# Optimization experiments

Measured on AMD Instinct MI355X. Metric: run time of the kernel, lower is better.

The kernel has to match this reference:

```python
import jax, jax.numpy as jnp
import numpy as np


def setup_inputs() -> dict:
    key = jax.random.key(0)
    k1, k2, k3 = jax.random.split(key, 3)
    B, C_IN, C_OUT, R, K = 4, 64, 64, 64, 3
    x = jax.random.normal(k1, (B, C_IN, R, R, R), dtype=jnp.float32)
    # per-voxel nonzero test |x|.sum(channel) != 0 used by the module)
    keep = jax.random.uniform(k2, (B, 1, R, R, R)) < 0.3
    x = x * keep.astype(jnp.float32)
    weight = jax.random.normal(k3, (C_OUT, C_IN, K, K, K), dtype=jnp.float32)
    return {"x": x, "weight": weight}


def reference(x, weight):
    # The torch module gathers a k^3 neighborhood at every nonzero input voxel,
    # contracts with the (unflipped) weight, and scatters to the same voxel.
    # This is exactly cross-correlation (torch conv semantics) with SAME padding,
    # masked to voxels where the input is nonzero across channels.
    K = weight.shape[-1]
    pad_l = K // 2
    pad_r = K - 1 - pad_l
    out = jax.lax.conv_general_dilated(
        x, weight,
        window_strides=(1, 1, 1),
        padding=[(pad_l, pad_r)] * 3,
        dimension_numbers=("NCDHW", "OIDHW", "NCDHW"),
    )  # [B, C_out, D, H, W]
    mask = (jnp.abs(x).sum(axis=1, keepdims=True) != 0)  # [B,1,D,H,W]
    return out * mask.astype(out.dtype)
```

## Files before the change

### kernel.cpp

```cpp
#include <hip/hip_runtime.h>
#include <stdint.h>


#define R3 262144
#define NVOX (4 * R3)
#define WSW_ELEMS (27 * 2 * 4 * 64 * 8)

typedef __attribute__((ext_vector_type(4))) float f32x4;
typedef __attribute__((ext_vector_type(8))) short short8;

static __device__ inline unsigned short f2bf(float f) {
    union { float f; unsigned u; } v; v.f = f;
    unsigned u = v.u;
    return (unsigned short)((u + 0x7fffu + ((u >> 16) & 1u)) >> 16);
}

__global__ void wprep(const float* __restrict__ w, unsigned short* __restrict__ wsw) {
    int e = blockIdx.x * 256 + threadIdx.x;
    if (e >= WSW_ELEMS) return;
    int j    = e & 7;
    int lane = (e >> 3) & 63;
    int nt   = (e >> 9) & 3;
    int kc   = (e >> 11) & 1;
    int tap  = e >> 12;
    int co = nt * 16 + (lane & 15);
    int ci = kc * 32 + ((lane >> 4) * 8) + j;
    wsw[e] = f2bf(w[(co * 64 + ci) * 27 + tap]);
}

__global__ void __launch_bounds__(256) xprep(const float* __restrict__ x,
                                             unsigned int* __restrict__ xt_u32,
                                             int* __restrict__ list,
                                             int* __restrict__ count) {
    __shared__ unsigned int lds[256 * 33];
    __shared__ unsigned int wcnt[4], wbase[4], bbase;
    int t = threadIdx.x;
    int v = blockIdx.x * 256 + t;
    int b = v >> 18;
    int s = v & (R3 - 1);
    const float* xb = x + (size_t)b * (64 * R3) + s;
    bool active = false;
#pragma unroll
    for (int c2 = 0; c2 < 32; ++c2) {
        float f0 = xb[(size_t)(2 * c2) * R3];
        float f1 = xb[(size_t)(2 * c2 + 1) * R3];
        active |= (f0 != 0.f) | (f1 != 0.f);
        lds[t * 33 + c2] = (unsigned)f2bf(f0) | ((unsigned)f2bf(f1) << 16);
    }
    __syncthreads();
    unsigned int* dst = xt_u32 + (size_t)blockIdx.x * 8192;
#pragma unroll
    for (int i = 0; i < 32; ++i) {
        int g = i * 256 + t;
        dst[g] = lds[(g >> 5) * 33 + (g & 31)];
    }
    int lane = t & 63, w = t >> 6;
    unsigned long long bal = __ballot(active);
    if (lane == 0) wcnt[w] = (unsigned)__popcll(bal);
    __syncthreads();
    if (t == 0) {
        unsigned tot = 0;
        for (int i = 0; i < 4; ++i) { wbase[i] = tot; tot += wcnt[i]; }
        bbase = (unsigned)atomicAdd(count, (int)tot);
    }
    __syncthreads();
    if (active) {
        unsigned pos = bbase + wbase[w] + (unsigned)__popcll(bal & ((1ULL << lane) - 1ULL));
        list[pos] = v;
    }
}

__global__ void __launch_bounds__(256) sconv_gemm(const unsigned short* __restrict__ xt,
                                                  const unsigned short* __restrict__ wsw,
                                                  const int* __restrict__ list,
                                                  const int* __restrict__ count_p,
                                                  float* __restrict__ out) {
    __shared__ __align__(16) unsigned short Alds[64 * 72];
    __shared__ int vids[64];
    int count = *count_p;
    int base = blockIdx.x * 64;
    if (base >= count) return;
    int t = threadIdx.x;
    if (t < 64) {
        int idx = base + t;
        vids[t] = (idx < count) ? list[idx] : -1;
    }
    __syncthreads();

    int lane = t & 63, w = t >> 6;
    int mt0 = (w & 1) * 2, nt0 = (w >> 1) * 2;
    f32x4 acc[2][2] = {};

    int srow = t >> 2;
    int scol = t & 3;
    int vid = vids[srow];
    bool vvalid = vid >= 0;
    int vx = vid & 63, vy = (vid >> 6) & 63, vz = (vid >> 12) & 63;
    int vbase = vid & ~(R3 - 1);

    for (int tap = 0; tap < 27; ++tap) {
        int dz = tap / 9 - 1, dy = (tap / 3) % 3 - 1, dx = tap % 3 - 1;
        uint4 val0 = {0, 0, 0, 0}, val1 = {0, 0, 0, 0};
        if (vvalid) {
            int nz = vz + dz, ny = vy + dy, nx = vx + dx;
            if ((unsigned)nz < 64u && (unsigned)ny < 64u && (unsigned)nx < 64u) {
                long long ns = (long long)vbase + nz * 4096 + ny * 64 + nx;
                const uint4* src = (const uint4*)(xt + (size_t)ns * 64) + scol * 2;
                val0 = src[0];
                val1 = src[1];
            }
        }
        *(uint4*)&Alds[srow * 72 + scol * 16] = val0;
        *(uint4*)&Alds[srow * 72 + scol * 16 + 8] = val1;
        __syncthreads();

#pragma unroll
        for (int kc = 0; kc < 2; ++kc) {
            short8 bfr[2], afr[2];
#pragma unroll
            for (int n = 0; n < 2; ++n) {
                int nt = nt0 + n;
                bfr[n] = *(const short8*)(wsw +
                          (((size_t)(tap * 8 + kc * 4 + nt)) * 64 + lane) * 8);
            }
#pragma unroll
            for (int m = 0; m < 2; ++m) {
                int row = (mt0 + m) * 16 + (lane & 15);
                afr[m] = *(const short8*)&Alds[row * 72 + kc * 32 + (lane >> 4) * 8];
            }
#pragma unroll
            for (int m = 0; m < 2; ++m)
#pragma unroll
                for (int n = 0; n < 2; ++n)
                    acc[m][n] = __builtin_amdgcn_mfma_f32_16x16x32_bf16(
                        afr[m], bfr[n], acc[m][n], 0, 0, 0);
        }
        __syncthreads();
    }

    int q = lane >> 4;
#pragma unroll
    for (int m = 0; m < 2; ++m) {
#pragma unroll
        for (int rg = 0; rg < 4; ++rg) {
            int row = (mt0 + m) * 16 + q * 4 + rg;
            if (base + row < count) {
                int vv = vids[row];
                int bb = vv >> 18;
                int sp = vv & (R3 - 1);
#pragma unroll
                for (int n = 0; n < 2; ++n) {
                    int co = (nt0 + n) * 16 + (lane & 15);
                    out[((size_t)(bb * 64 + co)) * R3 + sp] = acc[m][n][rg];
                }
            }
        }
    }
}

__global__ void __launch_bounds__(64) fallback_conv(const float* __restrict__ x,
                                                    const float* __restrict__ wt,
                                                    float* __restrict__ out) {
    __shared__ float rowb[66];
    int bid = blockIdx.x;
    int y = bid & 63, z = (bid >> 6) & 63, co = (bid >> 12) & 63, b = bid >> 18;
    int t = threadIdx.x;
    float acc = 0.f;
    bool active = false;
    for (int ci = 0; ci < 64; ++ci) {
        const float* xp = x + ((size_t)(b * 64 + ci)) * R3;
        const float* wp = wt + ((size_t)(co * 64 + ci)) * 27;
        for (int dz = -1; dz <= 1; ++dz) {
            int nz = z + dz;
            bool okz = (unsigned)nz < 64u;
            for (int dy = -1; dy <= 1; ++dy) {
                int ny = y + dy;
                bool ok = okz && ((unsigned)ny < 64u);
                float v = ok ? xp[nz * 4096 + ny * 64 + t] : 0.f;
                rowb[t + 1] = v;
                if (t == 0) { rowb[0] = 0.f; rowb[65] = 0.f; }
                __syncthreads();
                if (dz == 0 && dy == 0) active |= (rowb[t + 1] != 0.f);
                const float* wq = wp + (dz + 1) * 9 + (dy + 1) * 3;
                acc += rowb[t] * wq[0] + rowb[t + 1] * wq[1] + rowb[t + 2] * wq[2];
                __syncthreads();
            }
        }
    }
    out[((size_t)(b * 64 + co)) * R3 + z * 4096 + y * 64 + t] = active ? acc : 0.f;
}

extern "C" void kernel_launch(void* const* d_in, const int* in_sizes, int n_in,
                              void* d_out, int out_size, void* d_ws, size_t ws_size,
                              hipStream_t stream) {
    const float* x = (const float*)d_in[0];
    const float* w = (const float*)d_in[1];
    float* out = (float*)d_out;

    const size_t XT_BYTES  = (size_t)NVOX * 64 * 2;
    const size_t LIST_OFF  = XT_BYTES;
    const size_t WSW_OFF   = LIST_OFF + (size_t)NVOX * 4;
    const size_t CNT_OFF   = WSW_OFF + (size_t)WSW_ELEMS * 2;
    const size_t NEED      = CNT_OFF + 256;

    if (ws_size < NEED) {
        fallback_conv<<<NVOX, 64, 0, stream>>>(x, w, out);
        return;
    }

    unsigned int*   xt   = (unsigned int*)d_ws;
    int*            list = (int*)((char*)d_ws + LIST_OFF);
    unsigned short* wsw  = (unsigned short*)((char*)d_ws + WSW_OFF);
    int*            cnt  = (int*)((char*)d_ws + CNT_OFF);

    hipMemsetAsync(cnt, 0, sizeof(int), stream);
    hipMemsetAsync(d_out, 0, (size_t)out_size * sizeof(float), stream);
    wprep<<<WSW_ELEMS / 256, 256, 0, stream>>>(w, wsw);
    xprep<<<NVOX / 256, 256, 0, stream>>>(x, xt, list, cnt);
    sconv_gemm<<<NVOX / 64, 256, 0, stream>>>((const unsigned short*)xt, wsw, list, cnt, out);
}
```

Before: 710.8 us.

## Pad voxel grid with zero halo and double-buffer async LDS loads in sparse conv GEMM

Stores the bf16 channel-last input in a 66^3 zero-padded grid, adding a halo_zero kernel, so the gather needs no bounds checks. The GEMM kernel grows to 128 voxels per block with each warp covering all 64 output channels. It double-buffers the A and B tiles in LDS using global_load_lds with an XOR swizzle, so the next tap's loads overlap the current tap's MFMAs. This costs a larger workspace, an extra halo-zeroing pass, and more LDS per block.

```diff
diff --git a/kernel.cpp b/kernel.cpp
--- a/kernel.cpp
+++ b/kernel.cpp
@@ -4,6 +4,9 @@
 
 #define R3 262144
 #define NVOX (4 * R3)
+#define P  66
+#define PS (66 * 66)
+#define PB (66 * 66 * 66)
 #define WSW_ELEMS (27 * 2 * 4 * 64 * 8)
 
 typedef __attribute__((ext_vector_type(4))) float f32x4;
@@ -13,6 +16,12 @@
     union { float f; unsigned u; } v; v.f = f;
     unsigned u = v.u;
     return (unsigned short)((u + 0x7fffu + ((u >> 16) & 1u)) >> 16);
+}
+
+static __device__ __forceinline__ void gload16(const void* g, void* l) {
+    __builtin_amdgcn_global_load_lds(
+        (const __attribute__((address_space(1))) unsigned int*)g,
+        (__attribute__((address_space(3))) unsigned int*)l, 16, 0, 0);
 }
 
 __global__ void wprep(const float* __restrict__ w, unsigned short* __restrict__ wsw) {
@@ -28,11 +37,26 @@
     wsw[e] = f2bf(w[(co * 64 + ci) * 27 + tap]);
 }
 
+__global__ void __launch_bounds__(256) halo_zero(uint4* __restrict__ xt4) {
+    int p = blockIdx.x * 256 + threadIdx.x;
+    if (p >= 4 * PB) return;
+    int b = p / PB;
+    int rp = p - b * PB;
+    int z = rp / PS; rp -= z * PS;
+    int y = rp / P;  int xx = rp - y * P;
+    if (z == 0 || z == 65 || y == 0 || y == 65 || xx == 0 || xx == 65) {
+        uint4 zz = {0, 0, 0, 0};
+        uint4* d = xt4 + (size_t)p * 8;
+#pragma unroll
+        for (int k = 0; k < 8; ++k) d[k] = zz;
+    }
+}
+
 __global__ void __launch_bounds__(256) xprep(const float* __restrict__ x,
                                              unsigned int* __restrict__ xt_u32,
                                              int* __restrict__ list,
                                              int* __restrict__ count) {
-    __shared__ unsigned int lds[256 * 33];
+    __shared__ unsigned int lds[256 * 36];
     __shared__ unsigned int wcnt[4], wbase[4], bbase;
     int t = threadIdx.x;
     int v = blockIdx.x * 256 + t;
@@ -40,19 +64,33 @@
     int s = v & (R3 - 1);
     const float* xb = x + (size_t)b * (64 * R3) + s;
     bool active = false;
+    unsigned int pk[32];
 #pragma unroll
     for (int c2 = 0; c2 < 32; ++c2) {
         float f0 = xb[(size_t)(2 * c2) * R3];
         float f1 = xb[(size_t)(2 * c2 + 1) * R3];
         active |= (f0 != 0.f) | (f1 != 0.f);
-        lds[t * 33 + c2] = (unsigned)f2bf(f0) | ((unsigned)f2bf(f1) << 16);
-    }
-    __syncthreads();
-    unsigned int* dst = xt_u32 + (size_t)blockIdx.x * 8192;
-#pragma unroll
-    for (int i = 0; i < 32; ++i) {
-        int g = i * 256 + t;
-        dst[g] = lds[(g >> 5) * 33 + (g & 31)];
+        pk[c2] = (unsigned)f2bf(f0) | ((unsigned)f2bf(f1) << 16);
+    }
+#pragma unroll
+    for (int k = 0; k < 8; ++k) {
+        uint4 q = { pk[4 * k], pk[4 * k + 1], pk[4 * k + 2], pk[4 * k + 3] };
+        *(uint4*)&lds[t * 36 + 4 * k] = q;
+    }
+    __syncthreads();
+    int s0 = (blockIdx.x * 256) & (R3 - 1);
+    int z0 = s0 >> 12;
+    int y0 = (s0 >> 6) & 63;
+    size_t rowbase = ((size_t)b * PB + (size_t)(z0 + 1) * PS + (size_t)(y0 + 1) * P + 1) * 32;
+#pragma unroll
+    for (int i = 0; i < 8; ++i) {
+        int g4 = i * 256 + t;
+        int vox = g4 >> 3;
+        int col = (g4 & 7) * 4;
+        uint4 val = *(const uint4*)&lds[vox * 36 + col];
+        int r = vox >> 6;
+        int xc = vox & 63;
+        *(uint4*)&xt_u32[rowbase + (size_t)r * (P * 32) + (size_t)xc * 32 + col] = val;
     }
     int lane = t & 63, w = t >> 6;
     unsigned long long bal = __ballot(active);
@@ -70,72 +108,86 @@
     }
 }
 
-__global__ void __launch_bounds__(256) sconv_gemm(const unsigned short* __restrict__ xt,
-                                                  const unsigned short* __restrict__ wsw,
+#define STAGE(tap, buf) do {                                                       \
+    const int dz_ = (tap) / 9 - 1, dy_ = ((tap) / 3) % 3 - 1, dx_ = (tap) % 3 - 1; \
+    const ptrdiff_t dlt_ = (ptrdiff_t)(dz_ * PS + dy_ * P + dx_) * 128;            \
+    _Pragma("unroll")                                                              \
+    for (int i_ = 0; i_ < 4; ++i_)                                                 \
+        gload16(asrc[i_] + dlt_, &Ab[buf][(t + i_ * 256) * 16]);                   \
+    _Pragma("unroll")                                                              \
+    for (int i_ = 0; i_ < 2; ++i_)                                                 \
+        gload16(wswb + (size_t)(tap) * 8192 + (t + i_ * 256) * 16,                 \
+                &Bb[buf][(t + i_ * 256) * 16]);                                    \
+} while (0)
+
+__global__ void __launch_bounds__(256) sconv_gemm(const unsigned char* __restrict__ xt,
+                                                  const unsigned char* __restrict__ wswb,
                                                   const int* __restrict__ list,
                                                   const int* __restrict__ count_p,
                                                   float* __restrict__ out) {
-    __shared__ __align__(16) unsigned short Alds[64 * 72];
-    __shared__ int vids[64];
+    __shared__ __align__(16) unsigned char Ab[2][16384];
+    __shared__ __align__(16) unsigned char Bb[2][8192];
+    __shared__ int vids[128];
     int count = *count_p;
-    int base = blockIdx.x * 64;
+    int base = blockIdx.x * 128;
     if (base >= count) return;
     int t = threadIdx.x;
-    if (t < 64) {
-        int idx = base + t;
-        vids[t] = (idx < count) ? list[idx] : -1;
-    }
-    __syncthreads();
+    if (t < 128) { int idx = base + t; vids[t] = (idx < count) ? list[idx] : -1; }
+    __syncthreads();
+
+    const unsigned char* asrc[4];
+    {
+        int seg = t & 7;
+        int r0 = t >> 3;
+        int off = (seg * 16) ^ ((r0 & 7) << 4);
+#pragma unroll
+        for (int i = 0; i < 4; ++i) {
+            int vid = vids[r0 + 32 * i];
+            if (vid < 0) vid = 0;
+            int bb = vid >> 18, sp = vid & (R3 - 1);
+            int vz = sp >> 12, vy = (sp >> 6) & 63, vx = sp & 63;
+            size_t pvox = (size_t)bb * PB + (size_t)(vz + 1) * PS + (size_t)(vy + 1) * P + (vx + 1);
+            asrc[i] = xt + pvox * 128 + off;
+        }
+    }
 
     int lane = t & 63, w = t >> 6;
-    int mt0 = (w & 1) * 2, nt0 = (w >> 1) * 2;
-    f32x4 acc[2][2] = {};
-
-    int srow = t >> 2;
-    int scol = t & 3;
-    int vid = vids[srow];
-    bool vvalid = vid >= 0;
-    int vx = vid & 63, vy = (vid >> 6) & 63, vz = (vid >> 12) & 63;
-    int vbase = vid & ~(R3 - 1);
-
+    int cl = lane & 15;
+    int hi16 = (lane >> 4) * 16;
+    int aswz = (cl & 7) << 4;
+    int aoff[2][2];
+#pragma unroll
+    for (int m = 0; m < 2; ++m)
+#pragma unroll
+        for (int kc = 0; kc < 2; ++kc)
+            aoff[m][kc] = (w * 32 + m * 16 + cl) * 128 + ((kc * 64 + hi16) ^ aswz);
+    int boff[2][4];
+#pragma unroll
+    for (int kc = 0; kc < 2; ++kc)
+#pragma unroll
+        for (int n = 0; n < 4; ++n)
+            boff[kc][n] = ((kc * 4 + n) * 64 + lane) * 16;
+
+    f32x4 acc[2][4] = {};
+
+    STAGE(0, 0);
+    __syncthreads();
+#pragma unroll
     for (int tap = 0; tap < 27; ++tap) {
-        int dz = tap / 9 - 1, dy = (tap / 3) % 3 - 1, dx = tap % 3 - 1;
-        uint4 val0 = {0, 0, 0, 0}, val1 = {0, 0, 0, 0};
-        if (vvalid) {
-            int nz = vz + dz, ny = vy + dy, nx = vx + dx;
-            if ((unsigned)nz < 64u && (unsigned)ny < 64u && (unsigned)nx < 64u) {
-                long long ns = (long long)vbase + nz * 4096 + ny * 64 + nx;
-                const uint4* src = (const uint4*)(xt + (size_t)ns * 64) + scol * 2;
-                val0 = src[0];
-                val1 = src[1];
+        const int cur = tap & 1;
+        if (tap < 26) { STAGE(tap + 1, cur ^ 1); }
+#pragma unroll
+        for (int kc = 0; kc < 2; ++kc) {
+            short8 a0 = *(const short8*)&Ab[cur][aoff[0][kc]];
+            short8 a1 = *(const short8*)&Ab[cur][aoff[1][kc]];
+#pragma unroll
+            for (int n = 0; n < 4; ++n) {
+                short8 bf = *(const short8*)&Bb[cur][boff[kc][n]];
+                acc[0][n] = __builtin_amdgcn_mfma_f32_16x16x32_bf16(a0, bf, acc[0][n], 0, 0, 0);
+                acc[1][n] = __builtin_amdgcn_mfma_f32_16x16x32_bf16(a1, bf, acc[1][n], 0, 0, 0);
             }
         }
-        *(uint4*)&Alds[srow * 72 + scol * 16] = val0;
-        *(uint4*)&Alds[srow * 72 + scol * 16 + 8] = val1;
         __syncthreads();
-
-#pragma unroll
-        for (int kc = 0; kc < 2; ++kc) {
-            short8 bfr[2], afr[2];
-#pragma unroll
-            for (int n = 0; n < 2; ++n) {
-                int nt = nt0 + n;
-                bfr[n] = *(const short8*)(wsw +
-                          (((size_t)(tap * 8 + kc * 4 + nt)) * 64 + lane) * 8);
-            }
-#pragma unroll
-            for (int m = 0; m < 2; ++m) {
-                int row = (mt0 + m) * 16 + (lane & 15);
-                afr[m] = *(const short8*)&Alds[row * 72 + kc * 32 + (lane >> 4) * 8];
-            }
-#pragma unroll
-            for (int m = 0; m < 2; ++m)
-#pragma unroll
-                for (int n = 0; n < 2; ++n)
-                    acc[m][n] = __builtin_amdgcn_mfma_f32_16x16x32_bf16(
-                        afr[m], bfr[n], acc[m][n], 0, 0, 0);
-        }
-        __syncthreads();
     }
 
     int q = lane >> 4;
@@ -143,16 +195,15 @@
     for (int m = 0; m < 2; ++m) {
 #pragma unroll
         for (int rg = 0; rg < 4; ++rg) {
-            int row = (mt0 + m) * 16 + q * 4 + rg;
+            int row = w * 32 + m * 16 + q * 4 + rg;
             if (base + row < count) {
                 int vv = vids[row];
-                int bb = vv >> 18;
+                int bb2 = vv >> 18;
                 int sp = vv & (R3 - 1);
-#pragma unroll
-                for (int n = 0; n < 2; ++n) {
-                    int co = (nt0 + n) * 16 + (lane & 15);
-                    out[((size_t)(bb * 64 + co)) * R3 + sp] = acc[m][n][rg];
-                }
+                float* op = out + (size_t)(bb2 * 64 + cl) * R3 + sp;
+#pragma unroll
+                for (int n = 0; n < 4; ++n)
+                    op[(size_t)(n * 16) * R3] = acc[m][n][rg];
             }
         }
     }
@@ -197,11 +248,11 @@
     const float* w = (const float*)d_in[1];
     float* out = (float*)d_out;
 
-    const size_t XT_BYTES  = (size_t)NVOX * 64 * 2;
-    const size_t LIST_OFF  = XT_BYTES;
-    const size_t WSW_OFF   = LIST_OFF + (size_t)NVOX * 4;
-    const size_t CNT_OFF   = WSW_OFF + (size_t)WSW_ELEMS * 2;
-    const size_t NEED      = CNT_OFF + 256;
+    const size_t XT_BYTES = (size_t)4 * PB * 128;
+    const size_t LIST_OFF = XT_BYTES;
+    const size_t WSW_OFF  = LIST_OFF + (size_t)NVOX * 4;
+    const size_t CNT_OFF  = WSW_OFF + (size_t)WSW_ELEMS * 2;
+    const size_t NEED     = CNT_OFF + 256;
 
     if (ws_size < NEED) {
         fallback_conv<<<NVOX, 64, 0, stream>>>(x, w, out);
@@ -216,6 +267,8 @@
     hipMemsetAsync(cnt, 0, sizeof(int), stream);
     hipMemsetAsync(d_out, 0, (size_t)out_size * sizeof(float), stream);
     wprep<<<WSW_ELEMS / 256, 256, 0, stream>>>(w, wsw);
+    halo_zero<<<(4 * PB + 255) / 256, 256, 0, stream>>>((uint4*)d_ws);
     xprep<<<NVOX / 256, 256, 0, stream>>>(x, xt, list, cnt);
-    sconv_gemm<<<NVOX / 64, 256, 0, stream>>>((const unsigned short*)xt, wsw, list, cnt, out);
-}
+    sconv_gemm<<<NVOX / 128, 256, 0, stream>>>((const unsigned char*)xt,
+                                               (const unsigned char*)wsw, list, cnt, out);
+}
```

Result: slower. 748.9 us (+5.4%).
